# Optimization experiments

Measured on AMD Instinct MI355X. Metric: run time of the kernel, lower is better.

## Reference

```python
import jax, jax.numpy as jnp
import numpy as np

OUT_F, IN_F = 4096, 4096
GROUP = 128
NGROUPS = IN_F // GROUP  # 32


def setup_inputs() -> dict:
    key = jax.random.key(0)
    k1, k2, k3, k4 = jax.random.split(key, 4)
    x = jax.random.normal(k1, (4, 2048, IN_F), dtype=jnp.float32)
    # 4-bit codes stored as integers in [0, 16)
    compressed_weight = jax.random.randint(k2, (OUT_F, IN_F), 0, 16, dtype=jnp.int32)
    scale = jax.random.uniform(k3, (OUT_F, NGROUPS), dtype=jnp.float32)
    offset = jax.random.normal(k4, (OUT_F, NGROUPS), dtype=jnp.float32)
    return {"x": x, "compressed_weight": compressed_weight, "scale": scale, "offset": offset}


def reference(x, compressed_weight, scale, offset):
    # group-wise dequant: w[o, g, j] = code * scale[o, g] - offset[o, g]
    codes = compressed_weight.astype(scale.dtype).reshape(OUT_F, NGROUPS, GROUP)
    w = (codes * scale[..., None] - offset[..., None]).reshape(OUT_F, IN_F)
    # F.linear: x @ w.T  -> [B, S, OUT_F]
    return jnp.einsum('bsi,oi->bso', x, w.astype(x.dtype))
```

## Files before the change

kernel.cpp:

```cpp
#include <hip/hip_runtime.h>
#include <stdint.h>

#define OUT_F 4096
#define IN_F  4096
#define NGROUPS 32
#define BK 64
#define NT (IN_F / BK)

typedef __attribute__((ext_vector_type(4))) float    f32x4;
typedef __attribute__((ext_vector_type(8))) short    bf16x8;
typedef __attribute__((ext_vector_type(4))) int      i32x4;
typedef __attribute__((ext_vector_type(4))) uint32_t u32x4;

__device__ __forceinline__ ushort f2bf(float f) {
  union { float f; uint32_t u; } v; v.f = f;
  uint32_t r = v.u + 0x7FFFu + ((v.u >> 16) & 1u);
  return (ushort)(r >> 16);
}

__global__ void cvt_x_kernel(const float* __restrict__ x, ushort* __restrict__ xb, int n8) {
  int i = blockIdx.x * blockDim.x + threadIdx.x;
  if (i >= n8) return;
  const f32x4* xp = (const f32x4*)x;
  f32x4 a = xp[2 * i], b = xp[2 * i + 1];
  u32x4 o;
  o.x = (uint32_t)f2bf(a.x) | ((uint32_t)f2bf(a.y) << 16);
  o.y = (uint32_t)f2bf(a.z) | ((uint32_t)f2bf(a.w) << 16);
  o.z = (uint32_t)f2bf(b.x) | ((uint32_t)f2bf(b.y) << 16);
  o.w = (uint32_t)f2bf(b.z) | ((uint32_t)f2bf(b.w) << 16);
  ((u32x4*)xb)[i] = o;
}

__global__ void dequant_w_kernel(const int* __restrict__ cw,
                                 const float* __restrict__ sc,
                                 const float* __restrict__ of,
                                 ushort* __restrict__ wb) {
  int t = blockIdx.x * blockDim.x + threadIdx.x;
  int o  = t >> 9;
  int k0 = (t & 511) << 3;
  int g  = k0 >> 7;
  float s   = sc[o * NGROUPS + g];
  float off = of[o * NGROUPS + g];
  const i32x4* cp = (const i32x4*)(cw + (size_t)o * IN_F + k0);
  i32x4 c0 = cp[0], c1 = cp[1];
  u32x4 out;
  out.x = (uint32_t)f2bf((float)c0.x * s - off) | ((uint32_t)f2bf((float)c0.y * s - off) << 16);
  out.y = (uint32_t)f2bf((float)c0.z * s - off) | ((uint32_t)f2bf((float)c0.w * s - off) << 16);
  out.z = (uint32_t)f2bf((float)c1.x * s - off) | ((uint32_t)f2bf((float)c1.y * s - off) << 16);
  out.w = (uint32_t)f2bf((float)c1.z * s - off) | ((uint32_t)f2bf((float)c1.w * s - off) << 16);
  *(u32x4*)(wb + (size_t)o * IN_F + k0) = out;
}


#define BAR() do { asm volatile("" ::: "memory"); __builtin_amdgcn_s_barrier(); asm volatile("" ::: "memory"); } while (0)

#define GLLDS(gp, lp) __builtin_amdgcn_global_load_lds( \
  (const __attribute__((address_space(1))) uint32_t*)(const void*)(gp), \
  (__attribute__((address_space(3))) uint32_t*)(void*)(lp), 16, 0, 0)

#define STAGE_A(buf, kt) do { \
  _Pragma("unroll") for (int h_ = 0; h_ < 2; ++h_) \
  _Pragma("unroll") for (int c_ = 0; c_ < 2; ++c_) \
    GLLDS(A + (size_t)(m0 + h_ * 128 + c_ * 64 + stRow) * IN_F + (kt) * BK + sl * 8, \
          ldsb + (buf) * 65536 + h_ * 16384 + c_ * 8192 + wid * 1024); \
} while (0)

#define STAGE_B_HALF(buf, kt, h_) do { \
  _Pragma("unroll") for (int c_ = 0; c_ < 2; ++c_) \
    GLLDS(B + (size_t)(n0 + (h_) * 128 + c_ * 64 + stRow) * IN_F + (kt) * BK + sl * 8, \
          ldsb + (buf) * 65536 + 32768 + (h_) * 16384 + c_ * 8192 + wid * 1024); \
} while (0)

#define MFMA8(I0, J0) do { \
  _Pragma("unroll") for (int i_ = 0; i_ < 4; ++i_) \
  _Pragma("unroll") for (int j_ = 0; j_ < 2; ++j_) { \
    acc[(I0) + i_][(J0) + j_] = __builtin_amdgcn_mfma_f32_16x16x32_bf16(Ar[i_][0], Br[(J0) + j_][0], acc[(I0) + i_][(J0) + j_], 0, 0, 0); \
    acc[(I0) + i_][(J0) + j_] = __builtin_amdgcn_mfma_f32_16x16x32_bf16(Ar[i_][1], Br[(J0) + j_][1], acc[(I0) + i_][(J0) + j_], 0, 0, 0); \
  } } while (0)

__global__ __launch_bounds__(512, 2) void gemm256(const ushort* __restrict__ A,
                                                  const ushort* __restrict__ B,
                                                  float* __restrict__ C, int M) {
  __shared__ ushort lds[65536];
  char* ldsb = (char*)lds;

  const int nmt = M >> 8;
  const int nwg = gridDim.x;
  int wg = blockIdx.x;
  if ((nwg & 7) == 0) wg = (wg & 7) * (nwg >> 3) + (wg >> 3);
  const int bn = wg / nmt;
  const int bm = wg % nmt;
  const int m0 = bm << 8, n0 = bn << 8;

  const int tid  = threadIdx.x;
  const int lane = tid & 63;
  const int wid  = tid >> 6;
  const int wr   = wid >> 2;
  const int wc   = wid & 3;

  const int stRow = wid * 8 + (lane >> 3);
  const int sl    = (lane & 7) ^ (lane >> 3);

  const int frow = lane & 15;
  const int g    = lane >> 4;
  const int off0 = frow * 128 + (((g    ) ^ (lane & 7)) << 4);
  const int off1 = frow * 128 + (((4 + g) ^ (lane & 7)) << 4);

  f32x4 acc[8][4] = {};
  bf16x8 Ar[4][2], Br[4][2];

  STAGE_A(0, 0);
  STAGE_B_HALF(0, 0, 0);
  STAGE_B_HALF(0, 0, 1);
  STAGE_A(1, 1);
  asm volatile("s_waitcnt vmcnt(4)" ::: "memory");
  BAR();

#pragma unroll 1
  for (int t = 0; t < NT; ++t) {
    const int cur = t & 1, nxt = cur ^ 1;
    const char* aB = ldsb + cur * 65536 + wr * 16384;
    const char* bB = ldsb + cur * 65536 + 32768 + (wc >> 1) * 16384 + (wc & 1) * 8192;

#pragma unroll
    for (int i = 0; i < 4; ++i) {
      Ar[i][0] = *(const bf16x8*)(aB + i * 2048 + off0);
      Ar[i][1] = *(const bf16x8*)(aB + i * 2048 + off1);
    }
#pragma unroll
    for (int j = 0; j < 2; ++j) {
      Br[j][0] = *(const bf16x8*)(bB + j * 2048 + off0);
      Br[j][1] = *(const bf16x8*)(bB + j * 2048 + off1);
    }
    if (t + 1 < NT) STAGE_B_HALF(nxt, t + 1, 0);
    BAR();
    __builtin_amdgcn_s_setprio(1);
    MFMA8(0, 0);
    __builtin_amdgcn_s_setprio(0);
    BAR();

#pragma unroll
    for (int j = 2; j < 4; ++j) {
      Br[j][0] = *(const bf16x8*)(bB + j * 2048 + off0);
      Br[j][1] = *(const bf16x8*)(bB + j * 2048 + off1);
    }
    if (t + 1 < NT) STAGE_B_HALF(nxt, t + 1, 1);
    BAR();
    __builtin_amdgcn_s_setprio(1);
    MFMA8(0, 2);
    __builtin_amdgcn_s_setprio(0);
    BAR();

#pragma unroll
    for (int i = 0; i < 4; ++i) {
      Ar[i][0] = *(const bf16x8*)(aB + (4 + i) * 2048 + off0);
      Ar[i][1] = *(const bf16x8*)(aB + (4 + i) * 2048 + off1);
    }
    BAR();
    __builtin_amdgcn_s_setprio(1);
    MFMA8(4, 2);
    __builtin_amdgcn_s_setprio(0);
    BAR();

    if (t + 2 < NT) STAGE_A(cur, t + 2);
    BAR();
    __builtin_amdgcn_s_setprio(1);
    MFMA8(4, 0);
    __builtin_amdgcn_s_setprio(0);
    if (t + 2 < NT) { asm volatile("s_waitcnt vmcnt(4)" ::: "memory"); }
    else            { asm volatile("s_waitcnt vmcnt(0)" ::: "memory"); }
    BAR();
  }

  const int crow0 = m0 + wr * 128 + (g << 2);
  const int ccol0 = n0 + wc * 64 + frow;
#pragma unroll
  for (int mf = 0; mf < 8; ++mf)
#pragma unroll
    for (int nf = 0; nf < 4; ++nf)
#pragma unroll
      for (int q = 0; q < 4; ++q)
        C[(size_t)(crow0 + mf * 16 + q) * OUT_F + (ccol0 + nf * 16)] = acc[mf][nf][q];
}

__global__ void naive_kernel(const float* __restrict__ x, const int* __restrict__ cw,
                             const float* __restrict__ sc, const float* __restrict__ of,
                             float* __restrict__ out, int M) {
  int idx = blockIdx.x * blockDim.x + threadIdx.x;
  if (idx >= M * OUT_F) return;
  int o = idx & (OUT_F - 1);
  int m = idx >> 12;
  const float* xr = x + (size_t)m * IN_F;
  const int*   wr = cw + (size_t)o * IN_F;
  float acc = 0.f;
  for (int gg = 0; gg < NGROUPS; ++gg) {
    float s = sc[o * NGROUPS + gg], off = of[o * NGROUPS + gg];
#pragma unroll 8
    for (int k = 0; k < 128; ++k) {
      int kk = (gg << 7) + k;
      acc += xr[kk] * ((float)wr[kk] * s - off);
    }
  }
  out[idx] = acc;
}

extern "C" void kernel_launch(void* const* d_in, const int* in_sizes, int n_in,
                              void* d_out, int out_size, void* d_ws, size_t ws_size,
                              hipStream_t stream) {
  const float* x  = (const float*)d_in[0];
  const int*   cw = (const int*)d_in[1];
  const float* sc = (const float*)d_in[2];
  const float* of = (const float*)d_in[3];
  float* out = (float*)d_out;
  const int M = in_sizes[0] / IN_F;

  const size_t xb_bytes = (size_t)M * IN_F * 2;
  const size_t wb_bytes = (size_t)OUT_F * IN_F * 2;

  if (ws_size >= xb_bytes + wb_bytes && (M % 256) == 0) {
    ushort* xb = (ushort*)d_ws;
    ushort* wb = (ushort*)((char*)d_ws + xb_bytes);

    int n8 = (M * IN_F) / 8;
    cvt_x_kernel<<<(n8 + 255) / 256, 256, 0, stream>>>(x, xb, n8);

    int nw8 = (OUT_F * IN_F) / 8;
    dequant_w_kernel<<<(nw8 + 255) / 256, 256, 0, stream>>>(cw, sc, of, wb);

    dim3 grid((M / 256) * (OUT_F / 256));
    gemm256<<<grid, 512, 0, stream>>>(xb, wb, out, M);
  } else {
    int total = M * OUT_F;
    naive_kernel<<<(total + 255) / 256, 256, 0, stream>>>(x, cw, sc, of, out, M);
  }
}
```

Measured before the change: 300.9 us.

## Restructure GEMM main loop to prefetch A fragments and cut barriers

Reorganizes the per-tile schedule of the 256x256 bf16 GEMM. All B fragments are now loaded into two separate register sets up front. The second half of A is read earlier, and the first A fragments of the next k-tile are prefetched from LDS at the end of the current iteration. This drops the number of workgroup barriers per iteration from eight to five and lets LDS reads overlap more with MFMA work. In exchange it keeps more operand registers live, which raises VGPR pressure under the two-workgroup occupancy bound.

```diff
diff --git a/kernel.cpp b/kernel.cpp
--- a/kernel.cpp
+++ b/kernel.cpp
@@ -71,12 +71,27 @@
           ldsb + (buf) * 65536 + 32768 + (h_) * 16384 + c_ * 8192 + wid * 1024); \
 } while (0)
 
-#define MFMA8(I0, J0) do { \
+#define RD_A(base, i0) do { \
+  _Pragma("unroll") for (int i_ = 0; i_ < 4; ++i_) { \
+    Ar[i_][0] = *(const bf16x8*)((base) + ((i0) + i_) * 2048 + off0); \
+    Ar[i_][1] = *(const bf16x8*)((base) + ((i0) + i_) * 2048 + off1); \
+  } } while (0)
+
+#define RD_B(dst, j0) do { \
+  _Pragma("unroll") for (int j_ = 0; j_ < 2; ++j_) { \
+    dst[j_][0] = *(const bf16x8*)(bC + ((j0) + j_) * 2048 + off0); \
+    dst[j_][1] = *(const bf16x8*)(bC + ((j0) + j_) * 2048 + off1); \
+  } } while (0)
+
+#define MFMAQ(I0, J0, Bset) do { \
+  __builtin_amdgcn_s_setprio(1); \
   _Pragma("unroll") for (int i_ = 0; i_ < 4; ++i_) \
   _Pragma("unroll") for (int j_ = 0; j_ < 2; ++j_) { \
-    acc[(I0) + i_][(J0) + j_] = __builtin_amdgcn_mfma_f32_16x16x32_bf16(Ar[i_][0], Br[(J0) + j_][0], acc[(I0) + i_][(J0) + j_], 0, 0, 0); \
-    acc[(I0) + i_][(J0) + j_] = __builtin_amdgcn_mfma_f32_16x16x32_bf16(Ar[i_][1], Br[(J0) + j_][1], acc[(I0) + i_][(J0) + j_], 0, 0, 0); \
-  } } while (0)
+    acc[(I0) + i_][(J0) + j_] = __builtin_amdgcn_mfma_f32_16x16x32_bf16(Ar[i_][0], Bset[j_][0], acc[(I0) + i_][(J0) + j_], 0, 0, 0); \
+    acc[(I0) + i_][(J0) + j_] = __builtin_amdgcn_mfma_f32_16x16x32_bf16(Ar[i_][1], Bset[j_][1], acc[(I0) + i_][(J0) + j_], 0, 0, 0); \
+  } \
+  __builtin_amdgcn_s_setprio(0); \
+} while (0)
 
 __global__ __launch_bounds__(512, 2) void gemm256(const ushort* __restrict__ A,
                                                   const ushort* __restrict__ B,
@@ -107,7 +122,7 @@
   const int off1 = frow * 128 + (((4 + g) ^ (lane & 7)) << 4);
 
   f32x4 acc[8][4] = {};
-  bf16x8 Ar[4][2], Br[4][2];
+  bf16x8 Ar[4][2], Bl[2][2], Bh[2][2];
 
   STAGE_A(0, 0);
   STAGE_B_HALF(0, 0, 0);
@@ -115,60 +130,38 @@
   STAGE_A(1, 1);
   asm volatile("s_waitcnt vmcnt(4)" ::: "memory");
   BAR();
+  RD_A(ldsb + wr * 16384, 0);
 
 #pragma unroll 1
   for (int t = 0; t < NT; ++t) {
     const int cur = t & 1, nxt = cur ^ 1;
-    const char* aB = ldsb + cur * 65536 + wr * 16384;
-    const char* bB = ldsb + cur * 65536 + 32768 + (wc >> 1) * 16384 + (wc & 1) * 8192;
-
-#pragma unroll
-    for (int i = 0; i < 4; ++i) {
-      Ar[i][0] = *(const bf16x8*)(aB + i * 2048 + off0);
-      Ar[i][1] = *(const bf16x8*)(aB + i * 2048 + off1);
+    const char* aC = ldsb + cur * 65536 + wr * 16384;
+    const char* aN = ldsb + nxt * 65536 + wr * 16384;
+    const char* bC = ldsb + cur * 65536 + 32768 + (wc >> 1) * 16384 + (wc & 1) * 8192;
+
+    RD_B(Bl, 0);
+    RD_B(Bh, 2);
+    if (t + 1 < NT) STAGE_B_HALF(nxt, t + 1, 0);
+    BAR();
+    MFMAQ(0, 0, Bl);
+
+    if (t + 1 < NT) STAGE_B_HALF(nxt, t + 1, 1);
+    BAR();
+    MFMAQ(0, 2, Bh);
+    RD_A(aC, 4);
+    if (t + 1 < NT) { asm volatile("s_waitcnt vmcnt(4)" ::: "memory"); }
+    BAR();
+
+    MFMAQ(4, 2, Bh);
+    BAR();
+
+    if (t + 2 < NT) STAGE_A(cur, t + 2);
+    MFMAQ(4, 0, Bl);
+    if (t + 1 < NT) {
+      RD_A(aN, 0);
+      if (t + 2 < NT) { asm volatile("s_waitcnt vmcnt(4)" ::: "memory"); }
+      else            { asm volatile("s_waitcnt vmcnt(0)" ::: "memory"); }
     }
-#pragma unroll
-    for (int j = 0; j < 2; ++j) {
-      Br[j][0] = *(const bf16x8*)(bB + j * 2048 + off0);
-      Br[j][1] = *(const bf16x8*)(bB + j * 2048 + off1);
-    }
-    if (t + 1 < NT) STAGE_B_HALF(nxt, t + 1, 0);
-    BAR();
-    __builtin_amdgcn_s_setprio(1);
-    MFMA8(0, 0);
-    __builtin_amdgcn_s_setprio(0);
-    BAR();
-
-#pragma unroll
-    for (int j = 2; j < 4; ++j) {
-      Br[j][0] = *(const bf16x8*)(bB + j * 2048 + off0);
-      Br[j][1] = *(const bf16x8*)(bB + j * 2048 + off1);
-    }
-    if (t + 1 < NT) STAGE_B_HALF(nxt, t + 1, 1);
-    BAR();
-    __builtin_amdgcn_s_setprio(1);
-    MFMA8(0, 2);
-    __builtin_amdgcn_s_setprio(0);
-    BAR();
-
-#pragma unroll
-    for (int i = 0; i < 4; ++i) {
-      Ar[i][0] = *(const bf16x8*)(aB + (4 + i) * 2048 + off0);
-      Ar[i][1] = *(const bf16x8*)(aB + (4 + i) * 2048 + off1);
-    }
-    BAR();
-    __builtin_amdgcn_s_setprio(1);
-    MFMA8(4, 2);
-    __builtin_amdgcn_s_setprio(0);
-    BAR();
-
-    if (t + 2 < NT) STAGE_A(cur, t + 2);
-    BAR();
-    __builtin_amdgcn_s_setprio(1);
-    MFMA8(4, 0);
-    __builtin_amdgcn_s_setprio(0);
-    if (t + 2 < NT) { asm volatile("s_waitcnt vmcnt(4)" ::: "memory"); }
-    else            { asm volatile("s_waitcnt vmcnt(0)" ::: "memory"); }
     BAR();
   }
 
```

New measurement: 291.0 us. 3.3% less time.
